# Kernel optimization log

Hardware: AMD Instinct MI355X
Metric: run time of the kernel (lower is better)

The kernel has to match this reference:

```python
import jax, jax.numpy as jnp
import numpy as np
import math

NUM_HEADS = 8
HEAD_DIM = 64
MID = NUM_HEADS * HEAD_DIM  # 512
OUT_FEATURES = 512
NUM_BUCKETS = 32            # rel_pos_num_buckets (module passes 2*this to bucket fn)
MAX_DISTANCE = 128
SCALE = HEAD_DIM ** -0.5


def _relative_position_bucket(rel_pos, num_buckets, max_distance):
    # faithful port of RelativePositionBias._relative_position_bucket
    num_buckets = num_buckets // 2
    ret = (rel_pos >= 0).astype(jnp.int32) * num_buckets
    n = jnp.abs(rel_pos)
    max_exact = max(1, num_buckets // 2)
    denom = math.log(max_distance / max_exact) if max_distance > max_exact else 1.0
    n_float = jnp.maximum(n.astype(jnp.float32), 1.0)
    val_if_large = (max_exact + jnp.log(n_float / max_exact) / denom * (num_buckets - max_exact)).astype(jnp.int32)
    val_if_large = jnp.minimum(val_if_large, num_buckets - 1)
    ret = ret + jnp.where(n < max_exact, n, val_if_large)
    return ret


def rel_pos_bias(table, num_q, num_k):
    # table: [2*NUM_BUCKETS, heads] -> bias [1, heads, q, k]
    q_pos = jnp.arange(num_q, dtype=jnp.int32)
    k_pos = jnp.arange(num_k, dtype=jnp.int32)
    rel = k_pos[None, :] - q_pos[:, None]                      # [q, k]
    bucket = _relative_position_bucket(rel, NUM_BUCKETS * 2, MAX_DISTANCE)
    bias = table[bucket]                                       # [q, k, h]
    return jnp.transpose(bias, (2, 0, 1))[None]                # [1, h, q, k]


def setup_inputs() -> dict:
    key = jax.random.key(0)
    ks = jax.random.split(key, 6)
    b, n = 2, 4096
    q = jax.random.normal(ks[0], (b, n, MID), dtype=jnp.float32)
    k = jax.random.normal(ks[1], (b, n, MID), dtype=jnp.float32)
    v = jax.random.normal(ks[2], (b, n, MID), dtype=jnp.float32)
    # bucket indices range over [0, 2*NUM_BUCKETS); size table accordingly
    rel_bias_table = jax.random.normal(ks[3], (2 * NUM_BUCKETS, NUM_HEADS), dtype=jnp.float32) * 0.02
    W_out = jax.random.normal(ks[4], (MID, OUT_FEATURES), dtype=jnp.float32) * (1.0 / math.sqrt(MID))
    b_out = jax.random.normal(ks[5], (OUT_FEATURES,), dtype=jnp.float32) * 0.01
    return {"q": q, "k": k, "v": v, "rel_bias_table": rel_bias_table, "W_out": W_out, "b_out": b_out}


def reference(q, k, v, rel_bias_table, W_out, b_out):
    b, n, _ = q.shape
    m = k.shape[1]
    split = lambda t: jnp.transpose(t.reshape(t.shape[0], t.shape[1], NUM_HEADS, HEAD_DIM), (0, 2, 1, 3))
    qh, kh, vh = split(q), split(k), split(v)                  # [b, h, n, d]
    sim = jnp.einsum('bhnd,bhmd->bhnm', qh, kh)                # [b, h, n, m]
    sim = sim + rel_pos_bias(rel_bias_table, n, m)             # bias added BEFORE scaling (as in source)
    sim = sim * SCALE
    attn = jax.nn.softmax(sim, axis=-1)
    out = jnp.einsum('bhnm,bhmd->bhnd', attn, vh)              # [b, h, n, d]
    out = jnp.transpose(out, (0, 2, 1, 3)).reshape(b, n, MID)  # [b, n, h*d]
    return out @ W_out + b_out
```

## Files before the change

kernel.cpp:

```cpp
#include <hip/hip_runtime.h>
#include <hip/hip_bf16.h>
#include <math.h>

#define BB 2
#define HH 8
#define NN 4096
#define DD 64
#define MID 512
#define NOUT 512
#define QB 128
#define KVT 64
#define NT (NN / KVT)
#define LOG2E 1.44269504088896340736f
#define SCALE 0.125f

typedef __attribute__((ext_vector_type(8)))  short bf16x8;
typedef __attribute__((ext_vector_type(4)))  float f32x4;
typedef __attribute__((ext_vector_type(16))) float f32x16;

__device__ __forceinline__ short f2bf(float x) {
  unsigned u = __builtin_bit_cast(unsigned, x);
  u = (u + 0x7FFFu + ((u >> 16) & 1u)) >> 16;
  return (short)u;
}

__device__ __forceinline__ int rp_bucket(int rel) {
  int ret = (rel >= 0) ? 32 : 0;
  int n = (rel >= 0) ? rel : -rel;
  if (n < 16) return ret + n;
  float nf = (float)n;
  float vf = 16.0f + (logf(nf * (1.0f / 16.0f)) / 2.0794415416798357f) * 16.0f;
  int vi = (int)vf;
  vi = vi < 31 ? vi : 31;
  return ret + vi;
}

__device__ __forceinline__ unsigned cvtpk(float lo, float hi) {
  unsigned d;
  asm("v_cvt_pk_bf16_f32 %0, %1, %2" : "=v"(d) : "v"(lo), "v"(hi));
  return d;
}

__device__ __forceinline__ void gl2lds16(const void* g, void* l) {
  __builtin_amdgcn_global_load_lds(
      (const __attribute__((address_space(1))) unsigned*)g,
      (__attribute__((address_space(3))) unsigned*)l, 16, 0, 0);
}

__global__ __launch_bounds__(256) void prep_kernel(
    const float* __restrict__ W,  short* __restrict__ Wt,
    const float* __restrict__ K,  short* __restrict__ Kws,
    const float* __restrict__ V,  short* __restrict__ Vtws)
{
  const int bx = blockIdx.x;
  const int t  = threadIdx.x;
  if (bx < 2048) {
    int i = bx * 256 + t;
    int a = i & 7;
    int n = (i >> 3) & 4095;
    int h = (i >> 15) & 7;
    int b = i >> 18;
    const float* src = K + ((size_t)(b * 4096 + n) * 512 + h * 64 + a * 8);
    float4 x0 = *(const float4*)src;
    float4 x1 = *(const float4*)(src + 4);
    union { unsigned u[4]; bf16x8 v; } pk;
    pk.u[0] = cvtpk(x0.x, x0.y); pk.u[1] = cvtpk(x0.z, x0.w);
    pk.u[2] = cvtpk(x1.x, x1.y); pk.u[3] = cvtpk(x1.z, x1.w);
    size_t off = ((size_t)(b * 8 + h) * 4096 + n) * 64 + (size_t)((a ^ (n & 7)) * 8);
    *(bf16x8*)(Kws + off) = pk.v;
  } else if (bx < 2560) {
    __shared__ short Vl[2][64][72];
    const int idx = bx - 2048;
    const int g0 = (idx & 31) * 2;
    const int bh = idx >> 5;
    const int b = bh >> 3, h = bh & 7;
    const int c4 = t & 15, r = t >> 4;
    #pragma unroll
    for (int gg = 0; gg < 2; ++gg) {
      #pragma unroll
      for (int rr = 0; rr < 4; ++rr) {
        int nl = r + rr * 16;
        const float* src = V + ((size_t)(b * 4096 + (g0 + gg) * 64 + nl) * 512 + h * 64 + c4 * 4);
        float4 x = *(const float4*)src;
        unsigned lo = cvtpk(x.x, x.y), hi2 = cvtpk(x.z, x.w);
        unsigned* dst = (unsigned*)&Vl[gg][nl][c4 * 4];
        dst[0] = lo; dst[1] = hi2;
      }
    }
    __syncthreads();
    #pragma unroll
    for (int it = 0; it < 4; ++it) {
      int u = t + it * 256;
      int d = u >> 4, q4 = u & 15;
      int gg = q4 >> 3, sp = q4 & 7;
      int s = sp ^ (d & 7);
      union { short s[8]; bf16x8 v; } pk;
      #pragma unroll
      for (int e = 0; e < 8; ++e) {
        int np  = s * 8 + e;
        int p16 = np & 15;
        int kvl = (np & 48) | (4 * (p16 >> 3) + (p16 & 3) + 8 * ((p16 >> 2) & 1));
        pk.s[e] = Vl[gg][kvl][d];
      }
      *(bf16x8*)(Vtws + ((size_t)bh * 64 + d) * 4096 + (g0 + gg) * 64 + sp * 8) = pk.v;
    }
  } else {
    __shared__ short Wl[64][72];
    const int idx = bx - 2560;
    const int k0 = (idx & 7) * 64;
    const int n0 = (idx >> 3) * 64;
    const int c4 = t & 15, r = t >> 4;
    #pragma unroll
    for (int rr = 0; rr < 4; ++rr) {
      int kl = r + rr * 16;
      const float* src = W + (size_t)(k0 + kl) * 512 + n0 + c4 * 4;
      float4 x = *(const float4*)src;
      unsigned lo = cvtpk(x.x, x.y), hi2 = cvtpk(x.z, x.w);
      unsigned* dst = (unsigned*)&Wl[kl][c4 * 4];
      dst[0] = lo; dst[1] = hi2;
    }
    __syncthreads();
    #pragma unroll
    for (int it = 0; it < 2; ++it) {
      int u = t + it * 256;
      int nl = u >> 3, a = u & 7;
      union { short s[8]; bf16x8 v; } pk;
      #pragma unroll
      for (int e = 0; e < 8; ++e) pk.s[e] = Wl[a * 8 + e][nl];
      *(bf16x8*)(Wt + (size_t)(n0 + nl) * 512 + k0 + a * 8) = pk.v;
    }
  }
}

__global__ __launch_bounds__(256, 2) void attn_kernel(
    const float* __restrict__ q, const short* __restrict__ kws,
    const short* __restrict__ vtws, const float* __restrict__ table,
    short* __restrict__ attn_out)
{
  __shared__ short Ks[3][4096];
  __shared__ short Vs[3][4096];
  __shared__ float biasb[512];
  __shared__ float Lw[4][32];

  const int tid = threadIdx.x;
  const int w   = tid >> 6;
  const int l   = tid & 63;
  const int lq  = l & 31;
  const int hi  = l >> 5;

  const int raw = blockIdx.x;
  const int bh  = (raw & 7) * 2 + (raw >> 8);
  const int xb  = (raw >> 3) & 31;
  const int b = bh >> 3, h = bh & 7;
  const int q0 = xb * QB;
  const int qw = q0 + w * 32;
  const int qg = qw + lq;

  const float smul = SCALE * LOG2E;

  for (int i = tid; i < 512; i += 256)
    biasb[i] = table[rp_bucket(i - 256) * HH + h] * smul;
  const float c_lo = table[31 * HH + h] * smul;
  const float c_hi = table[63 * HH + h] * smul;

  f32x16 c16h, c16l;
  #pragma unroll
  for (int r = 0; r < 16; ++r) { c16h[r] = c_hi; c16l[r] = c_lo; }

  bf16x8 qf[4];
  {
    const float* qr = q + ((size_t)b * NN + qg) * MID + (size_t)h * DD;
    #pragma unroll
    for (int dc = 0; dc < 4; ++dc) {
      int d0 = dc * 16 + hi * 8;
      float4 a0 = *(const float4*)(qr + d0);
      float4 a1 = *(const float4*)(qr + d0 + 4);
      bf16x8 f;
      f[0] = f2bf(a0.x * smul); f[1] = f2bf(a0.y * smul);
      f[2] = f2bf(a0.z * smul); f[3] = f2bf(a0.w * smul);
      f[4] = f2bf(a1.x * smul); f[5] = f2bf(a1.y * smul);
      f[6] = f2bf(a1.z * smul); f[7] = f2bf(a1.w * smul);
      qf[dc] = f;
    }
  }

  const short* kbh = kws  + (size_t)bh * NN * DD;
  const short* vbh = vtws + (size_t)bh * DD * NN;

  f32x16 o0a = {}, o0b = {}, o1a = {}, o1b = {};
  float ls0 = 0.f, ls1 = 0.f, ls2 = 0.f, ls3 = 0.f;

  const int o1w = w * 1024 + l * 16;
  const int o2w = o1w + 4096;
  const char* pkA = (const char*)kbh + o1w;
  const char* pvA = (const char*)vbh + (size_t)(o1w >> 7) * 8192 + (o1w & 127);
  const char* pvB = (const char*)vbh + (size_t)(o2w >> 7) * 8192 + (o2w & 127);
  char* ldsK = (char*)&Ks[0][0] + w * 1024;
  char* ldsV = (char*)&Vs[0][0] + w * 1024;
  const char* kbase = (const char*)&Ks[0][0];
  const char* vbase = (const char*)&Vs[0][0];

#define STAGE(BOFF) {                                   \
    gl2lds16(pkA,        ldsK + (BOFF));                \
    gl2lds16(pkA + 4096, ldsK + (BOFF) + 4096);         \
    gl2lds16(pvA,        ldsV + (BOFF));                \
    gl2lds16(pvB,        ldsV + (BOFF) + 4096);         \
    pkA += 8192; pvA += 128; pvB += 128; }

  __syncthreads();
  STAGE(0);
  STAGE(8192);

  int bo_cur = 0, bo_nxt = 16384;

  for (int t = 0; t < NT; ++t) {
    if (t + 1 < NT) asm volatile("s_waitcnt vmcnt(4)" ::: "memory");
    else            asm volatile("s_waitcnt vmcnt(0)" ::: "memory");
    __builtin_amdgcn_s_barrier();

    const int kv0 = t * KVT;

    const char* kr0 = kbase + bo_cur + lq * 128;
    const char* kr1 = kr0 + 32 * 128;
    const int swz = lq & 7;
    bf16x8 kf00 = *(const bf16x8*)(kr0 + ((hi ^ swz) << 4));
    bf16x8 kf10 = *(const bf16x8*)(kr1 + ((hi ^ swz) << 4));

    const int lo_rel = kv0 - (qw + 31);
    const int hi_rel = kv0 + KVT - 1 - qw;
    f32x16 acc0, acc1;
    if (lo_rel > 127) {
      acc0 = __builtin_amdgcn_mfma_f32_32x32x16_bf16(kf00, qf[0], c16h, 0, 0, 0);
      acc1 = __builtin_amdgcn_mfma_f32_32x32x16_bf16(kf10, qf[0], c16h, 0, 0, 0);
    } else if (hi_rel < -127) {
      acc0 = __builtin_amdgcn_mfma_f32_32x32x16_bf16(kf00, qf[0], c16l, 0, 0, 0);
      acc1 = __builtin_amdgcn_mfma_f32_32x32x16_bf16(kf10, qf[0], c16l, 0, 0, 0);
    } else {
      const int bidx0 = kv0 - qg + 256;
      f32x16 g0, g1;
      #pragma unroll
      for (int r = 0; r < 16; ++r) {
        int cr = (r & 3) + 8 * (r >> 2) + 4 * hi;
        g0[r] = biasb[bidx0 + cr];
        g1[r] = biasb[bidx0 + 32 + cr];
      }
      acc0 = __builtin_amdgcn_mfma_f32_32x32x16_bf16(kf00, qf[0], g0, 0, 0, 0);
      acc1 = __builtin_amdgcn_mfma_f32_32x32x16_bf16(kf10, qf[0], g1, 0, 0, 0);
    }
    __builtin_amdgcn_s_setprio(1);
    #pragma unroll
    for (int dc = 1; dc < 4; ++dc) {
      bf16x8 kf0 = *(const bf16x8*)(kr0 + (((dc * 2 + hi) ^ swz) << 4));
      bf16x8 kf1 = *(const bf16x8*)(kr1 + (((dc * 2 + hi) ^ swz) << 4));
      acc0 = __builtin_amdgcn_mfma_f32_32x32x16_bf16(kf0, qf[dc], acc0, 0, 0, 0);
      acc1 = __builtin_amdgcn_mfma_f32_32x32x16_bf16(kf1, qf[dc], acc1, 0, 0, 0);
    }
    __builtin_amdgcn_s_setprio(0);

    float p0[16], p1[16];
    #pragma unroll
    for (int r = 0; r < 16; ++r) p0[r] = __builtin_amdgcn_exp2f(acc0[r]);
    #pragma unroll
    for (int r = 0; r < 16; ++r) p1[r] = __builtin_amdgcn_exp2f(acc1[r]);

    ls0 += ((p0[0] + p0[1]) + (p0[2] + p0[3])) + ((p0[4] + p0[5]) + (p0[6] + p0[7]));
    ls1 += ((p0[8] + p0[9]) + (p0[10] + p0[11])) + ((p0[12] + p0[13]) + (p0[14] + p0[15]));
    ls2 += ((p1[0] + p1[1]) + (p1[2] + p1[3])) + ((p1[4] + p1[5]) + (p1[6] + p1[7]));
    ls3 += ((p1[8] + p1[9]) + (p1[10] + p1[11])) + ((p1[12] + p1[13]) + (p1[14] + p1[15]));

    bf16x8 pa[4];
    {
      union { unsigned u[4]; bf16x8 v; } ua, ub, uc, ud;
      ua.u[0] = cvtpk(p0[0],  p0[1]);  ua.u[1] = cvtpk(p0[2],  p0[3]);
      ua.u[2] = cvtpk(p0[4],  p0[5]);  ua.u[3] = cvtpk(p0[6],  p0[7]);
      ub.u[0] = cvtpk(p0[8],  p0[9]);  ub.u[1] = cvtpk(p0[10], p0[11]);
      ub.u[2] = cvtpk(p0[12], p0[13]); ub.u[3] = cvtpk(p0[14], p0[15]);
      uc.u[0] = cvtpk(p1[0],  p1[1]);  uc.u[1] = cvtpk(p1[2],  p1[3]);
      uc.u[2] = cvtpk(p1[4],  p1[5]);  uc.u[3] = cvtpk(p1[6],  p1[7]);
      ud.u[0] = cvtpk(p1[8],  p1[9]);  ud.u[1] = cvtpk(p1[10], p1[11]);
      ud.u[2] = cvtpk(p1[12], p1[13]); ud.u[3] = cvtpk(p1[14], p1[15]);
      pa[0] = ua.v; pa[1] = ub.v; pa[2] = uc.v; pa[3] = ud.v;
    }

    {
      const char* vr0 = vbase + bo_cur + lq * 128;
      const char* vr1 = vr0 + 32 * 128;
      const int s0 = lq & 7;
      __builtin_amdgcn_s_setprio(1);
      #pragma unroll
      for (int ks = 0; ks < 4; ks += 2) {
        bf16x8 vfa0 = *(const bf16x8*)(vr0 + (((hi + 2 * ks) ^ s0) << 4));
        bf16x8 vfb0 = *(const bf16x8*)(vr0 + (((hi + 2 * (ks + 1)) ^ s0) << 4));
        bf16x8 vfa1 = *(const bf16x8*)(vr1 + (((hi + 2 * ks) ^ s0) << 4));
        bf16x8 vfb1 = *(const bf16x8*)(vr1 + (((hi + 2 * (ks + 1)) ^ s0) << 4));
        o0a = __builtin_amdgcn_mfma_f32_32x32x16_bf16(pa[ks],     vfa0, o0a, 0, 0, 0);
        o0b = __builtin_amdgcn_mfma_f32_32x32x16_bf16(pa[ks + 1], vfb0, o0b, 0, 0, 0);
        o1a = __builtin_amdgcn_mfma_f32_32x32x16_bf16(pa[ks],     vfa1, o1a, 0, 0, 0);
        o1b = __builtin_amdgcn_mfma_f32_32x32x16_bf16(pa[ks + 1], vfb1, o1b, 0, 0, 0);
      }
      __builtin_amdgcn_s_setprio(0);
    }

    if (t + 2 < NT) STAGE(bo_nxt);
    bo_cur = (bo_cur == 16384) ? 0 : bo_cur + 8192;
    bo_nxt = (bo_nxt == 16384) ? 0 : bo_nxt + 8192;
  }

  f32x16 o0, o1;
  #pragma unroll
  for (int r = 0; r < 16; ++r) { o0[r] = o0a[r] + o0b[r]; o1[r] = o1a[r] + o1b[r]; }
  float lsum = (ls0 + ls1) + (ls2 + ls3);
  float tot = lsum + __shfl_xor(lsum, 32);
  if (l < 32) Lw[w][l] = tot;
  __syncthreads();
  float inv[16];
  #pragma unroll
  for (int g = 0; g < 4; ++g) {
    f32x4 t4 = *(const f32x4*)&Lw[w][g * 8 + hi * 4];
    inv[g * 4 + 0] = 1.0f / t4[0];
    inv[g * 4 + 1] = 1.0f / t4[1];
    inv[g * 4 + 2] = 1.0f / t4[2];
    inv[g * 4 + 3] = 1.0f / t4[3];
  }
  const size_t ob = ((size_t)b * NN + qw) * MID + (size_t)h * DD;
  #pragma unroll
  for (int r = 0; r < 16; ++r) {
    const int crow = (r & 3) + 8 * (r >> 2) + 4 * hi;
    short* orow = attn_out + ob + (size_t)crow * MID;
    orow[lq]      = f2bf(o0[r] * inv[r]);
    orow[32 + lq] = f2bf(o1[r] * inv[r]);
  }
#undef STAGE
}

__global__ __launch_bounds__(256) void proj_kernel(
    const short* __restrict__ A, const short* __restrict__ Wt,
    const float* __restrict__ bias, float* __restrict__ out)
{
  const int tid = threadIdx.x;
  const int w  = tid >> 6;
  const int l  = tid & 63;
  const int lr = l & 15;
  const int lg = l >> 4;
  const int bid = blockIdx.x;
  const int mp = (bid & 7) * 8 + ((bid >> 3) & 7);
  const int n0 = (bid >> 6) * 64;
  const int m0 = mp * 128 + w * 16;
  const int m1 = m0 + 64;

  f32x4 acc0[4] = {}, acc1[4] = {};
  const short* ar0 = A + (size_t)(m0 + lr) * MID + lg * 8;
  const short* ar1 = A + (size_t)(m1 + lr) * MID + lg * 8;
  #pragma unroll
  for (int kk = 0; kk < MID; kk += 32) {
    bf16x8 af0 = *(const bf16x8*)(ar0 + kk);
    bf16x8 af1 = *(const bf16x8*)(ar1 + kk);
    #pragma unroll
    for (int u = 0; u < 4; ++u) {
      bf16x8 bfr = *(const bf16x8*)(Wt + (size_t)(n0 + u * 16 + lr) * MID + kk + lg * 8);
      acc0[u] = __builtin_amdgcn_mfma_f32_16x16x32_bf16(af0, bfr, acc0[u], 0, 0, 0);
      acc1[u] = __builtin_amdgcn_mfma_f32_16x16x32_bf16(af1, bfr, acc1[u], 0, 0, 0);
    }
  }
  #pragma unroll
  for (int u = 0; u < 4; ++u) {
    float bb = bias[n0 + u * 16 + lr];
    #pragma unroll
    for (int r = 0; r < 4; ++r) {
      out[(size_t)(m0 + lg * 4 + r) * NOUT + n0 + u * 16 + lr] = acc0[u][r] + bb;
      out[(size_t)(m1 + lg * 4 + r) * NOUT + n0 + u * 16 + lr] = acc1[u][r] + bb;
    }
  }
}

extern "C" void kernel_launch(void* const* d_in, const int* in_sizes, int n_in,
                              void* d_out, int out_size, void* d_ws, size_t ws_size,
                              hipStream_t stream) {
  const float* q     = (const float*)d_in[0];
  const float* k     = (const float*)d_in[1];
  const float* v     = (const float*)d_in[2];
  const float* table = (const float*)d_in[3];
  const float* W     = (const float*)d_in[4];
  const float* bo    = (const float*)d_in[5];
  float* out = (float*)d_out;

  char* wsp = (char*)d_ws;
  short* attn_ws = (short*)wsp;                       wsp += (size_t)BB * NN * MID * 2;
  short* Wt      = (short*)wsp;                       wsp += (size_t)MID * NOUT * 2;
  short* kws     = (short*)wsp;                       wsp += (size_t)BB * HH * NN * DD * 2;
  short* vtws    = (short*)wsp;

  hipLaunchKernelGGL(prep_kernel, dim3(2624), dim3(256), 0, stream,
                     W, Wt, k, kws, v, vtws);
  hipLaunchKernelGGL(attn_kernel, dim3(BB * HH * (NN / QB)), dim3(256), 0, stream,
                     q, kws, vtws, table, attn_ws);
  hipLaunchKernelGGL(proj_kernel, dim3(512), dim3(256), 0, stream,
                     attn_ws, Wt, bo, out);
}
```

Before: 121.6 us.

## Split KV range across two wave groups per block with LDS output merge

The attention block doubles to 512 threads. Two groups of four waves each process alternating 64-key halves of a 128-key tile for the same query rows, and their partial outputs and row sums are combined through LDS at the end. Staging moves from a triple-buffered, two-tile-ahead prefetch to a double-buffered one-ahead prefetch with a full vmcnt(0) wait each iteration. This aims to raise the number of waves per CU and halve the serial loop length, but it adds a final LDS reduction and barrier and loses prefetch depth.

New measurement: 407.7 us. 235% more time.

```diff
diff --git a/kernel.cpp b/kernel.cpp
--- a/kernel.cpp
+++ b/kernel.cpp
@@ -9,8 +9,7 @@
 #define MID 512
 #define NOUT 512
 #define QB 128
-#define KVT 64
-#define NT (NN / KVT)
+#define NR 32
 #define LOG2E 1.44269504088896340736f
 #define SCALE 0.125f
 
@@ -132,34 +131,35 @@
   }
 }
 
-__global__ __launch_bounds__(256, 2) void attn_kernel(
+__global__ __launch_bounds__(512, 4) void attn_kernel(
     const float* __restrict__ q, const short* __restrict__ kws,
     const short* __restrict__ vtws, const float* __restrict__ table,
     short* __restrict__ attn_out)
 {
-  __shared__ short Ks[3][4096];
-  __shared__ short Vs[3][4096];
+  __shared__ short Ks[2][2][4096];
+  __shared__ short Vs[2][2][4096];
   __shared__ float biasb[512];
-  __shared__ float Lw[4][32];
+  __shared__ float Lw[8][32];
 
   const int tid = threadIdx.x;
   const int w   = tid >> 6;
   const int l   = tid & 63;
   const int lq  = l & 31;
   const int hi  = l >> 5;
+  const int pg  = w >> 2;
+  const int ws  = w & 3;
 
   const int raw = blockIdx.x;
   const int bh  = (raw & 7) * 2 + (raw >> 8);
   const int xb  = (raw >> 3) & 31;
   const int b = bh >> 3, h = bh & 7;
   const int q0 = xb * QB;
-  const int qw = q0 + w * 32;
+  const int qw = q0 + ws * 32;
   const int qg = qw + lq;
 
   const float smul = SCALE * LOG2E;
 
-  for (int i = tid; i < 512; i += 256)
-    biasb[i] = table[rp_bucket(i - 256) * HH + h] * smul;
+  biasb[tid] = table[rp_bucket(tid - 256) * HH + h] * smul;
   const float c_lo = table[31 * HH + h] * smul;
   const float c_hi = table[63 * HH + h] * smul;
 
@@ -190,44 +190,39 @@
   f32x16 o0a = {}, o0b = {}, o1a = {}, o1b = {};
   float ls0 = 0.f, ls1 = 0.f, ls2 = 0.f, ls3 = 0.f;
 
-  const int o1w = w * 1024 + l * 16;
-  const int o2w = o1w + 4096;
-  const char* pkA = (const char*)kbh + o1w;
-  const char* pvA = (const char*)vbh + (size_t)(o1w >> 7) * 8192 + (o1w & 127);
-  const char* pvB = (const char*)vbh + (size_t)(o2w >> 7) * 8192 + (o2w & 127);
-  char* ldsK = (char*)&Ks[0][0] + w * 1024;
-  char* ldsV = (char*)&Vs[0][0] + w * 1024;
-  const char* kbase = (const char*)&Ks[0][0];
-  const char* vbase = (const char*)&Vs[0][0];
+  const int vo = tid * 16;
+  const char* pkA = (const char*)kbh + vo;
+  const char* pvA = (const char*)vbh + (size_t)(vo >> 7) * 8192 + (vo & 127);
+  char* ldsK = (char*)&Ks[0][0][0] + vo;
+  char* ldsV = (char*)&Vs[0][0][0] + vo;
+  const char* kbase = (const char*)&Ks[0][0][0];
+  const char* vbase = (const char*)&Vs[0][0][0];
+  const int swz = lq & 7;
 
 #define STAGE(BOFF) {                                   \
     gl2lds16(pkA,        ldsK + (BOFF));                \
-    gl2lds16(pkA + 4096, ldsK + (BOFF) + 4096);         \
+    gl2lds16(pkA + 8192, ldsK + (BOFF) + 8192);         \
     gl2lds16(pvA,        ldsV + (BOFF));                \
-    gl2lds16(pvB,        ldsV + (BOFF) + 4096);         \
-    pkA += 8192; pvA += 128; pvB += 128; }
-
-  __syncthreads();
+    gl2lds16(pvA + 128,  ldsV + (BOFF) + 8192);         \
+    pkA += 16384; pvA += 256; }
+
   STAGE(0);
-  STAGE(8192);
-
-  int bo_cur = 0, bo_nxt = 16384;
-
-  for (int t = 0; t < NT; ++t) {
-    if (t + 1 < NT) asm volatile("s_waitcnt vmcnt(4)" ::: "memory");
-    else            asm volatile("s_waitcnt vmcnt(0)" ::: "memory");
+
+  for (int t = 0; t < NR; ++t) {
+    asm volatile("s_waitcnt vmcnt(0)" ::: "memory");
     __builtin_amdgcn_s_barrier();
-
-    const int kv0 = t * KVT;
-
-    const char* kr0 = kbase + bo_cur + lq * 128;
+    if (t + 1 < NR) STAGE(((t + 1) & 1) * 16384);
+
+    const int bo  = (t & 1) * 16384 + pg * 8192;
+    const int kv0 = t * 128 + pg * 64;
+
+    const char* kr0 = kbase + bo + lq * 128;
     const char* kr1 = kr0 + 32 * 128;
-    const int swz = lq & 7;
     bf16x8 kf00 = *(const bf16x8*)(kr0 + ((hi ^ swz) << 4));
     bf16x8 kf10 = *(const bf16x8*)(kr1 + ((hi ^ swz) << 4));
 
     const int lo_rel = kv0 - (qw + 31);
-    const int hi_rel = kv0 + KVT - 1 - qw;
+    const int hi_rel = kv0 + 63 - qw;
     f32x16 acc0, acc1;
     if (lo_rel > 127) {
       acc0 = __builtin_amdgcn_mfma_f32_32x32x16_bf16(kf00, qf[0], c16h, 0, 0, 0);
@@ -283,16 +278,15 @@
     }
 
     {
-      const char* vr0 = vbase + bo_cur + lq * 128;
+      const char* vr0 = vbase + bo + lq * 128;
       const char* vr1 = vr0 + 32 * 128;
-      const int s0 = lq & 7;
       __builtin_amdgcn_s_setprio(1);
       #pragma unroll
       for (int ks = 0; ks < 4; ks += 2) {
-        bf16x8 vfa0 = *(const bf16x8*)(vr0 + (((hi + 2 * ks) ^ s0) << 4));
-        bf16x8 vfb0 = *(const bf16x8*)(vr0 + (((hi + 2 * (ks + 1)) ^ s0) << 4));
-        bf16x8 vfa1 = *(const bf16x8*)(vr1 + (((hi + 2 * ks) ^ s0) << 4));
-        bf16x8 vfb1 = *(const bf16x8*)(vr1 + (((hi + 2 * (ks + 1)) ^ s0) << 4));
+        bf16x8 vfa0 = *(const bf16x8*)(vr0 + (((hi + 2 * ks) ^ swz) << 4));
+        bf16x8 vfb0 = *(const bf16x8*)(vr0 + (((hi + 2 * (ks + 1)) ^ swz) << 4));
+        bf16x8 vfa1 = *(const bf16x8*)(vr1 + (((hi + 2 * ks) ^ swz) << 4));
+        bf16x8 vfb1 = *(const bf16x8*)(vr1 + (((hi + 2 * (ks + 1)) ^ swz) << 4));
         o0a = __builtin_amdgcn_mfma_f32_32x32x16_bf16(pa[ks],     vfa0, o0a, 0, 0, 0);
         o0b = __builtin_amdgcn_mfma_f32_32x32x16_bf16(pa[ks + 1], vfb0, o0b, 0, 0, 0);
         o1a = __builtin_amdgcn_mfma_f32_32x32x16_bf16(pa[ks],     vfa1, o1a, 0, 0, 0);
@@ -300,10 +294,6 @@
       }
       __builtin_amdgcn_s_setprio(0);
     }
-
-    if (t + 2 < NT) STAGE(bo_nxt);
-    bo_cur = (bo_cur == 16384) ? 0 : bo_cur + 8192;
-    bo_nxt = (bo_nxt == 16384) ? 0 : bo_nxt + 8192;
   }
 
   f32x16 o0, o1;
@@ -313,22 +303,38 @@
   float tot = lsum + __shfl_xor(lsum, 32);
   if (l < 32) Lw[w][l] = tot;
   __syncthreads();
-  float inv[16];
-  #pragma unroll
-  for (int g = 0; g < 4; ++g) {
-    f32x4 t4 = *(const f32x4*)&Lw[w][g * 8 + hi * 4];
-    inv[g * 4 + 0] = 1.0f / t4[0];
-    inv[g * 4 + 1] = 1.0f / t4[1];
-    inv[g * 4 + 2] = 1.0f / t4[2];
-    inv[g * 4 + 3] = 1.0f / t4[3];
-  }
-  const size_t ob = ((size_t)b * NN + qw) * MID + (size_t)h * DD;
-  #pragma unroll
-  for (int r = 0; r < 16; ++r) {
-    const int crow = (r & 3) + 8 * (r >> 2) + 4 * hi;
-    short* orow = attn_out + ob + (size_t)crow * MID;
-    orow[lq]      = f2bf(o0[r] * inv[r]);
-    orow[32 + lq] = f2bf(o1[r] * inv[r]);
+
+  float* Olds = (float*)&Ks[0][0][0];
+  if (pg == 1) {
+    float* ob = Olds + ws * 2048;
+    #pragma unroll
+    for (int r = 0; r < 16; ++r) {
+      const int crow = (r & 3) + 8 * (r >> 2) + 4 * hi;
+      ob[crow * 64 + lq]      = o0[r];
+      ob[crow * 64 + 32 + lq] = o1[r];
+    }
+  }
+  __syncthreads();
+  if (pg == 0) {
+    float inv[16];
+    #pragma unroll
+    for (int gq = 0; gq < 4; ++gq) {
+      f32x4 ta = *(const f32x4*)&Lw[w][gq * 8 + hi * 4];
+      f32x4 tb = *(const f32x4*)&Lw[w + 4][gq * 8 + hi * 4];
+      inv[gq * 4 + 0] = 1.0f / (ta[0] + tb[0]);
+      inv[gq * 4 + 1] = 1.0f / (ta[1] + tb[1]);
+      inv[gq * 4 + 2] = 1.0f / (ta[2] + tb[2]);
+      inv[gq * 4 + 3] = 1.0f / (ta[3] + tb[3]);
+    }
+    const float* ob = Olds + ws * 2048;
+    const size_t obase = ((size_t)b * NN + qw) * MID + (size_t)h * DD;
+    #pragma unroll
+    for (int r = 0; r < 16; ++r) {
+      const int crow = (r & 3) + 8 * (r >> 2) + 4 * hi;
+      short* orow = attn_out + obase + (size_t)crow * MID;
+      orow[lq]      = f2bf((o0[r] + ob[crow * 64 + lq])      * inv[r]);
+      orow[32 + lq] = f2bf((o1[r] + ob[crow * 64 + 32 + lq]) * inv[r]);
+    }
   }
 #undef STAGE
 }
@@ -392,7 +398,7 @@
 
   hipLaunchKernelGGL(prep_kernel, dim3(2624), dim3(256), 0, stream,
                      W, Wt, k, kws, v, vtws);
-  hipLaunchKernelGGL(attn_kernel, dim3(BB * HH * (NN / QB)), dim3(256), 0, stream,
+  hipLaunchKernelGGL(attn_kernel, dim3(BB * HH * (NN / QB)), dim3(512), 0, stream,
                      q, kws, vtws, table, attn_ws);
   hipLaunchKernelGGL(proj_kernel, dim3(512), dim3(256), 0, stream,
                      attn_ws, Wt, bo, out);
```
